# Kernel optimization log

Hardware: AMD Instinct MI355X
Metric: run time of the kernel (lower is better)

The kernel has to match this reference:

```python
import jax, jax.numpy as jnp
import numpy as np

# Directional rectangle cumulative max: max over the axis-aligned rectangle
# between each pixel and one image corner.

def _rectmax(x, rev_h, rev_w):
    y = jax.lax.cummax(x, axis=2, reverse=rev_h)
    return jax.lax.cummax(y, axis=3, reverse=rev_w)


def _guided_pool(xq, gq, rev_h, rev_w):
    # Guided landmark pool: each pixel takes max of itself and the directional
    # cumulative max restricted to guide==1 positions. With guide == ones this
    # reduces to the plain directional rectangle cummax (the un-guided pool).
    neg = jnp.finfo(xq.dtype).min
    masked = jnp.where(gq > 0, xq, neg)
    return jnp.maximum(xq, _rectmax(masked, rev_h, rev_w))

# (rev_h, rev_w) for TopLeft, TopRight, BottomLeft, BottomRight pools
_DIRS = [(True, True), (True, False), (False, True), (False, False)]


def setup_inputs() -> dict:
    key = jax.random.key(0)
    k1, k2, k3 = jax.random.split(key, 3)
    B, C, H, W = 16, 256, 64, 64
    Cout, K = 256, 3
    x = jax.random.normal(k1, (B, C, H, W), jnp.float32)
    weight = jax.random.normal(k2, (Cout, C, K, K), jnp.float32) * 0.02
    bias = jax.random.normal(k3, (Cout,), jnp.float32) * 0.02
    return {"x": x, "weight": weight, "bias": bias}


def reference(x, weight, bias):
    B, C, H, W = x.shape
    Q = C // 4
    # Original torch code squares x IN PLACE via chunk() views before pooling.
    xsq = x * x
    # Per-quadrant channel energy and its global (row, col) argmax -> one-hot guide.
    energy = xsq.reshape(B, 4, Q, H, W).sum(axis=2)            # [B,4,H,W]
    idx = jnp.argmax(energy.reshape(B, 4, H * W), axis=-1)     # [B,4]
    onehot = (jnp.arange(H * W) == idx[..., None]).astype(x.dtype)
    guide = jnp.broadcast_to(onehot.reshape(B, 4, 1, H, W), (B, 4, Q, H, W)).reshape(B, C, H, W)
    # Four directional guided pools, one per channel quadrant, then conv.
    xs = jnp.split(xsq, 4, axis=1)
    gs = jnp.split(guide, 4, axis=1)
    pooled = jnp.concatenate(
        [_guided_pool(xs[i], gs[i], *_DIRS[i]) for i in range(4)], axis=1)
    out = jax.lax.conv_general_dilated(
        pooled, weight, window_strides=(1, 1), padding='SAME',
        dimension_numbers=('NCHW', 'OIHW', 'NCHW'))
    return out + bias[None, :, None, None]
```

## Files before the change

### kernel.cpp

```cpp
#include <hip/hip_runtime.h>
#include <cstddef>

#define B_   16
#define C_   256
#define HW_  4096

typedef __attribute__((ext_vector_type(8)))  short bf16x8;
typedef __attribute__((ext_vector_type(16))) float f32x16;

static __device__ __forceinline__ unsigned short f2bf(float f) {
    unsigned int u = __float_as_uint(f);
    u += 0x7fffu + ((u >> 16) & 1u);
    return (unsigned short)(u >> 16);
}

__global__ __launch_bounds__(256) void fused_energy(const float* __restrict__ x,
                                                    unsigned short* __restrict__ xsqN,
                                                    float* __restrict__ pval,
                                                    int* __restrict__ pidx) {
    int blk = blockIdx.x;
    int b = blk >> 6, h = blk & 63;
    int tid = threadIdx.x;
    int w = tid & 63, layer = tid >> 6;
    __shared__ float earr[4][4][64];
    __shared__ unsigned short tile[64][264];
    float e0 = 0.f, e1 = 0.f, e2 = 0.f, e3 = 0.f;
    const float* xb = x + (size_t)b * C_ * HW_ + h * 64 + w;
#pragma unroll
    for (int i = 0; i < 8; ++i) {
        int c0 = (i * 4 + layer) * 8;
        union { unsigned short us[8]; int4 v; } u;
        float es = 0.f;
#pragma unroll
        for (int k = 0; k < 8; ++k) {
            float v = xb[(size_t)(c0 + k) * HW_];
            float s = v * v;
            es += s;
            u.us[k] = f2bf(s);
        }
        *(int4*)&tile[w][c0] = u.v;
        if ((i >> 1) == 0) e0 += es;
        else if ((i >> 1) == 1) e1 += es;
        else if ((i >> 1) == 2) e2 += es;
        else e3 += es;
    }
    earr[layer][0][w] = e0; earr[layer][1][w] = e1;
    earr[layer][2][w] = e2; earr[layer][3][w] = e3;
    __syncthreads();
    size_t base = (size_t)(b * 64 + h) * 64 * 256;
#pragma unroll
    for (int it = 0; it < 8; ++it) {
        int row  = it * 8 + (tid >> 5);
        int col8 = (tid & 31) * 8;
        *(int4*)(xsqN + base + (size_t)row * 256 + col8) = *(int4*)&tile[row][col8];
    }
    int q = tid >> 6;
    float ev = earr[0][q][w] + earr[1][q][w] + earr[2][q][w] + earr[3][q][w];
    int ix = h * 64 + w;
#pragma unroll
    for (int off = 32; off; off >>= 1) {
        float ov = __shfl_down(ev, off);
        int   oi = __shfl_down(ix, off);
        if (ov > ev || (ov == ev && oi < ix)) { ev = ov; ix = oi; }
    }
    if ((tid & 63) == 0) {
        pval[(b * 64 + h) * 4 + q] = ev;
        pidx[(b * 64 + h) * 4 + q] = ix;
    }
}

__global__ __launch_bounds__(64) void energy_final(const float* __restrict__ pval,
                                                   const int* __restrict__ pidx,
                                                   int* __restrict__ lm) {
    int bq = blockIdx.x;
    int b = bq >> 2, q = bq & 3;
    int h = threadIdx.x;
    float ev = pval[(b * 64 + h) * 4 + q];
    int   ix = pidx[(b * 64 + h) * 4 + q];
#pragma unroll
    for (int off = 32; off; off >>= 1) {
        float ov = __shfl_down(ev, off);
        int   oi = __shfl_down(ix, off);
        if (ov > ev || (ov == ev && oi < ix)) { ev = ov; ix = oi; }
    }
    if (h == 0) lm[bq] = ix;
}

__global__ __launch_bounds__(256) void lval_kernel(const unsigned short* __restrict__ xsqN,
                                                   const int* __restrict__ lm,
                                                   unsigned short* __restrict__ Lval) {
    int t = blockIdx.x * 256 + threadIdx.x;
    int b = t >> 8, c = t & 255, q = c >> 6;
    int l = lm[b * 4 + q];
    Lval[t] = xsqN[((size_t)((b * 64 + (l >> 6)) * 64 + (l & 63))) * 256 + c];
}

__global__ __launch_bounds__(64) void wt_pack(const float* __restrict__ w,
                                              unsigned short* __restrict__ wa) {
    int blk  = blockIdx.x;
    int lane = threadIdx.x;
    int cog = blk & 7;
    int s   = (blk >> 3) & 1;
    int cib = (blk >> 4) & 7;
    int j   = blk >> 7;
    int co  = cog * 32 + (lane & 31);
    int k0  = cib * 32 + s * 16 + (lane >> 5) * 8;
    union { unsigned short us[8]; int4 v; } u;
#pragma unroll
    for (int jj = 0; jj < 8; ++jj) {
        int ci = k0 + jj;
        u.us[jj] = f2bf(w[(size_t)(co * 256 + ci) * 9 + j]);
    }
    *(int4*)(wa + ((size_t)blk * 64 + lane) * 8) = u.v;
}

__global__ __launch_bounds__(512, 2) void conv_mfma(const unsigned short* __restrict__ xsqN,
                                                    const unsigned short* __restrict__ wa,
                                                    const float* __restrict__ bias,
                                                    const int* __restrict__ lm,
                                                    const unsigned short* __restrict__ Lval,
                                                    float* __restrict__ out) {
    int pt = blockIdx.x;
    int b  = pt >> 4;
    int h0 = (pt & 15) * 4;
    int tid  = threadIdx.x;
    int lane = tid & 63;
    int wv   = tid >> 6;
    int wy = wv >> 2, wx = wv & 3;
    int l31 = lane & 31, qh = lane >> 5;

    __shared__ unsigned short Bs[2][6 * 66 * 40];
    __shared__ unsigned short As[2][8192];

    f32x16 acc[4][2];
#pragma unroll
    for (int mt = 0; mt < 4; ++mt)
#pragma unroll
        for (int nt = 0; nt < 2; ++nt)
#pragma unroll
            for (int r = 0; r < 16; ++r) acc[mt][nt][r] = 0.f;

    int4 sv[4];
    int4 av0, av1;

    {
#pragma unroll
        for (int t2 = 0; t2 < 4; ++t2) {
            int idx = tid + t2 * 512;
            int4 v = {0, 0, 0, 0};
            if (idx < 1584) {
                int pr = idx / 264; int rem = idx - pr * 264;
                int pc = rem >> 2;  int part = rem & 3;
                int grow = h0 - 1 + pr, gcol = pc - 1;
                if ((unsigned)grow < 64u && (unsigned)gcol < 64u)
                    v = *(const int4*)(xsqN + (((size_t)(b * 64 + grow) * 64 + gcol) * 256 + part * 8));
            }
            sv[t2] = v;
        }
        int l = lm[b * 4 + 0];
        int hm = l >> 6, wm = l & 63;
#pragma unroll
        for (int t2 = 0; t2 < 4; ++t2) {
            int idx = tid + t2 * 512;
            if (idx < 1584) {
                int pr = idx / 264; int rem = idx - pr * 264;
                int pc = rem >> 2;  int part = rem & 3;
                int grow = h0 - 1 + pr, gcol = pc - 1;
                union { int4 v; unsigned short us[8]; } u; u.v = sv[t2];
                bool inb = ((unsigned)grow < 64u) && ((unsigned)gcol < 64u);
                if (inb && grow <= hm && gcol <= wm) {
                    union { int4 v; unsigned short us[8]; } Lu;
                    Lu.v = *(const int4*)(Lval + b * 256 + part * 8);
#pragma unroll
                    for (int k = 0; k < 8; ++k)
                        if (Lu.us[k] > u.us[k]) u.us[k] = Lu.us[k];
                }
                *(int4*)(&Bs[0][(pr * 66 + pc) * 40 + part * 8]) = u.v;
            }
        }
        const unsigned short* src = wa + tid * 16;
        av0 = *(const int4*)src;
        av1 = *(const int4*)(src + 8);
        *(int4*)(&As[0][tid * 16])     = av0;
        *(int4*)(&As[0][tid * 16 + 8]) = av1;
    }
    __syncthreads();

    for (int cib = 0; cib < 8; ++cib) {
        for (int j = 0; j < 9; ++j) {
            int p = cib * 9 + j;
            bool hasNext = (p < 71);
            if (hasNext) {
                int jn = j + 1, cibn = cib;
                if (jn == 9) { jn = 0; cibn = cib + 1; }
                const unsigned short* src = wa + ((size_t)(jn * 8 + cibn) << 13) + tid * 16;
                av0 = *(const int4*)src;
                av1 = *(const int4*)(src + 8);
            }
            if (j == 0 && cib < 7) {
                int nc = cib + 1;
#pragma unroll
                for (int t2 = 0; t2 < 4; ++t2) {
                    int idx = tid + t2 * 512;
                    int4 v = {0, 0, 0, 0};
                    if (idx < 1584) {
                        int pr = idx / 264; int rem = idx - pr * 264;
                        int pc = rem >> 2;  int part = rem & 3;
                        int grow = h0 - 1 + pr, gcol = pc - 1;
                        if ((unsigned)grow < 64u && (unsigned)gcol < 64u)
                            v = *(const int4*)(xsqN + (((size_t)(b * 64 + grow) * 64 + gcol) * 256 + nc * 32 + part * 8));
                    }
                    sv[t2] = v;
                }
            }

            {
                const unsigned short* Ab = &As[p & 1][0];
                const unsigned short* Bb = &Bs[cib & 1][0];
                int dh = j / 3 - 1, dw = j % 3 - 1;
                int r  = wx + dh + 1;
                int w0 = l31 + dw + 1;
#pragma unroll
                for (int s = 0; s < 2; ++s) {
                    const bf16x8* ap = (const bf16x8*)(Ab + (((s * 8 + wy * 4) * 64 + lane) << 3));
                    bf16x8 a0 = ap[0];
                    bf16x8 a1 = ap[64];
                    bf16x8 a2 = ap[128];
                    bf16x8 a3 = ap[192];
                    bf16x8 b0 = *(const bf16x8*)(Bb + (r * 66 + w0) * 40 + s * 16 + qh * 8);
                    bf16x8 b1 = *(const bf16x8*)(Bb + (r * 66 + w0 + 32) * 40 + s * 16 + qh * 8);
                    acc[0][0] = __builtin_amdgcn_mfma_f32_32x32x16_bf16(a0, b0, acc[0][0], 0, 0, 0);
                    acc[0][1] = __builtin_amdgcn_mfma_f32_32x32x16_bf16(a0, b1, acc[0][1], 0, 0, 0);
                    acc[1][0] = __builtin_amdgcn_mfma_f32_32x32x16_bf16(a1, b0, acc[1][0], 0, 0, 0);
                    acc[1][1] = __builtin_amdgcn_mfma_f32_32x32x16_bf16(a1, b1, acc[1][1], 0, 0, 0);
                    acc[2][0] = __builtin_amdgcn_mfma_f32_32x32x16_bf16(a2, b0, acc[2][0], 0, 0, 0);
                    acc[2][1] = __builtin_amdgcn_mfma_f32_32x32x16_bf16(a2, b1, acc[2][1], 0, 0, 0);
                    acc[3][0] = __builtin_amdgcn_mfma_f32_32x32x16_bf16(a3, b0, acc[3][0], 0, 0, 0);
                    acc[3][1] = __builtin_amdgcn_mfma_f32_32x32x16_bf16(a3, b1, acc[3][1], 0, 0, 0);
                }
            }

            if (j == 8 && cib < 7) {
                int nc = cib + 1;
                int l = lm[b * 4 + (nc >> 1)];
                int hm = l >> 6, wm = l & 63;
                bool qhle = (nc >> 1) < 2;
                bool qwle = ((nc >> 1) & 1) == 0;
                unsigned short* Bw = &Bs[(cib + 1) & 1][0];
#pragma unroll
                for (int t2 = 0; t2 < 4; ++t2) {
                    int idx = tid + t2 * 512;
                    if (idx < 1584) {
                        int pr = idx / 264; int rem = idx - pr * 264;
                        int pc = rem >> 2;  int part = rem & 3;
                        int grow = h0 - 1 + pr, gcol = pc - 1;
                        union { int4 v; unsigned short us[8]; } u; u.v = sv[t2];
                        bool inb = ((unsigned)grow < 64u) && ((unsigned)gcol < 64u);
                        bool hok = qhle ? (grow <= hm) : (grow >= hm);
                        bool wok = qwle ? (gcol <= wm) : (gcol >= wm);
                        if (inb && hok && wok) {
                            union { int4 v; unsigned short us[8]; } Lu;
                            Lu.v = *(const int4*)(Lval + b * 256 + nc * 32 + part * 8);
#pragma unroll
                            for (int k = 0; k < 8; ++k)
                                if (Lu.us[k] > u.us[k]) u.us[k] = Lu.us[k];
                        }
                        *(int4*)(&Bw[(pr * 66 + pc) * 40 + part * 8]) = u.v;
                    }
                }
            }
            if (hasNext) {
                unsigned short* dst = &As[(p + 1) & 1][tid * 16];
                *(int4*)dst       = av0;
                *(int4*)(dst + 8) = av1;
            }
            __syncthreads();
        }
    }

    int h = h0 + wx;
#pragma unroll
    for (int mt = 0; mt < 4; ++mt) {
#pragma unroll
        for (int nt = 0; nt < 2; ++nt) {
#pragma unroll
            for (int r = 0; r < 16; ++r) {
                int row = (r & 3) + 8 * (r >> 2) + 4 * qh;
                int co  = wy * 128 + mt * 32 + row;
                int w   = nt * 32 + l31;
                out[(((size_t)(b * 256 + co)) * 64 + h) * 64 + w] = acc[mt][nt][r] + bias[co];
            }
        }
    }
}

extern "C" void kernel_launch(void* const* d_in, const int* in_sizes, int n_in,
                              void* d_out, int out_size, void* d_ws, size_t ws_size,
                              hipStream_t stream) {
    const float* x      = (const float*)d_in[0];
    const float* weight = (const float*)d_in[1];
    const float* bias   = (const float*)d_in[2];
    float* out = (float*)d_out;

    char* ws = (char*)d_ws;
    int*            lmp  = (int*)ws;
    float*          pval = (float*)(ws + 256);
    int*            pidx = (int*)(ws + 256 + 16384);
    unsigned short* Lval = (unsigned short*)(ws + 256 + 32768);
    unsigned short* Wa   = (unsigned short*)(ws + 49152);
    unsigned short* xsqN = (unsigned short*)(ws + 49152 + 1179648);

    hipLaunchKernelGGL(fused_energy, dim3(1024), dim3(256), 0, stream, x, xsqN, pval, pidx);
    hipLaunchKernelGGL(energy_final, dim3(64), dim3(64), 0, stream, pval, pidx, lmp);
    hipLaunchKernelGGL(lval_kernel, dim3(16), dim3(256), 0, stream, xsqN, lmp, Lval);
    hipLaunchKernelGGL(wt_pack, dim3(1152), dim3(64), 0, stream, weight, Wa);
    hipLaunchKernelGGL(conv_mfma, dim3(256), dim3(512), 0, stream, xsqN, Wa, bias, lmp, Lval, out);
}
```

Before: 198.5 us.

## Retile conv to 8-row blocks with weights in registers and fewer barriers

Restructures the implicit-GEMM conv so each block covers 8 image rows and half the output channels. Each of 4 waves computes a 128x128 tile (4x4 MFMA accumulators), and the A (weight) fragments are read directly from global memory into registers with one-step prefetch instead of being staged through LDS. The 9 taps per channel block now run without a barrier between them, leaving one __syncthreads per channel block rather than one per tap. The lval kernel is also folded into energy_final to save a launch. In exchange the kernel needs more registers per wave and a larger LDS halo buffer, and runs at 256 threads with launch bounds for one block per SIMD, which lowers occupancy.

```diff
diff --git a/kernel.cpp b/kernel.cpp
--- a/kernel.cpp
+++ b/kernel.cpp
@@ -71,28 +71,25 @@
 
 __global__ __launch_bounds__(64) void energy_final(const float* __restrict__ pval,
                                                    const int* __restrict__ pidx,
-                                                   int* __restrict__ lm) {
+                                                   const unsigned short* __restrict__ xsqN,
+                                                   int* __restrict__ lm,
+                                                   unsigned short* __restrict__ Lval) {
     int bq = blockIdx.x;
     int b = bq >> 2, q = bq & 3;
-    int h = threadIdx.x;
-    float ev = pval[(b * 64 + h) * 4 + q];
-    int   ix = pidx[(b * 64 + h) * 4 + q];
+    int t = threadIdx.x;
+    float ev = pval[(b * 64 + t) * 4 + q];
+    int   ix = pidx[(b * 64 + t) * 4 + q];
 #pragma unroll
     for (int off = 32; off; off >>= 1) {
         float ov = __shfl_down(ev, off);
         int   oi = __shfl_down(ix, off);
         if (ov > ev || (ov == ev && oi < ix)) { ev = ov; ix = oi; }
     }
-    if (h == 0) lm[bq] = ix;
-}
-
-__global__ __launch_bounds__(256) void lval_kernel(const unsigned short* __restrict__ xsqN,
-                                                   const int* __restrict__ lm,
-                                                   unsigned short* __restrict__ Lval) {
-    int t = blockIdx.x * 256 + threadIdx.x;
-    int b = t >> 8, c = t & 255, q = c >> 6;
-    int l = lm[b * 4 + q];
-    Lval[t] = xsqN[((size_t)((b * 64 + (l >> 6)) * 64 + (l & 63))) * 256 + c];
+    int ixw = __shfl(ix, 0);
+    if (t == 0) lm[bq] = ixw;
+    int hm = ixw >> 6, wm = ixw & 63;
+    Lval[b * 256 + q * 64 + t] =
+        xsqN[((size_t)((b * 64 + hm) * 64 + wm)) * 256 + q * 64 + t];
 }
 
 __global__ __launch_bounds__(64) void wt_pack(const float* __restrict__ w,
@@ -114,44 +111,44 @@
     *(int4*)(wa + ((size_t)blk * 64 + lane) * 8) = u.v;
 }
 
-__global__ __launch_bounds__(512, 2) void conv_mfma(const unsigned short* __restrict__ xsqN,
+__global__ __launch_bounds__(256, 1) void conv_mfma(const unsigned short* __restrict__ xsqN,
                                                     const unsigned short* __restrict__ wa,
                                                     const float* __restrict__ bias,
                                                     const int* __restrict__ lm,
                                                     const unsigned short* __restrict__ Lval,
                                                     float* __restrict__ out) {
     int pt = blockIdx.x;
-    int b  = pt >> 4;
-    int h0 = (pt & 15) * 4;
+    int b   = pt >> 4;
+    int hb  = (pt >> 1) & 7;
+    int wy  = pt & 1;
+    int h0g = hb * 8;
     int tid  = threadIdx.x;
     int lane = tid & 63;
-    int wv   = tid >> 6;
-    int wy = wv >> 2, wx = wv & 3;
+    int wx   = tid >> 6;
     int l31 = lane & 31, qh = lane >> 5;
 
-    __shared__ unsigned short Bs[2][6 * 66 * 40];
-    __shared__ unsigned short As[2][8192];
-
-    f32x16 acc[4][2];
+    __shared__ unsigned short Bs[2][26400];
+
+    f32x16 acc[4][4];
 #pragma unroll
     for (int mt = 0; mt < 4; ++mt)
 #pragma unroll
-        for (int nt = 0; nt < 2; ++nt)
+        for (int nt = 0; nt < 4; ++nt)
 #pragma unroll
             for (int r = 0; r < 16; ++r) acc[mt][nt][r] = 0.f;
 
-    int4 sv[4];
-    int4 av0, av1;
+    int4 sv[11];
+    int4 aC[8], aN[8];
 
     {
 #pragma unroll
-        for (int t2 = 0; t2 < 4; ++t2) {
-            int idx = tid + t2 * 512;
+        for (int t2 = 0; t2 < 11; ++t2) {
+            int idx = tid + t2 * 256;
             int4 v = {0, 0, 0, 0};
-            if (idx < 1584) {
+            if (idx < 2640) {
                 int pr = idx / 264; int rem = idx - pr * 264;
                 int pc = rem >> 2;  int part = rem & 3;
-                int grow = h0 - 1 + pr, gcol = pc - 1;
+                int grow = h0g - 1 + pr, gcol = pc - 1;
                 if ((unsigned)grow < 64u && (unsigned)gcol < 64u)
                     v = *(const int4*)(xsqN + (((size_t)(b * 64 + grow) * 64 + gcol) * 256 + part * 8));
             }
@@ -160,12 +157,12 @@
         int l = lm[b * 4 + 0];
         int hm = l >> 6, wm = l & 63;
 #pragma unroll
-        for (int t2 = 0; t2 < 4; ++t2) {
-            int idx = tid + t2 * 512;
-            if (idx < 1584) {
+        for (int t2 = 0; t2 < 11; ++t2) {
+            int idx = tid + t2 * 256;
+            if (idx < 2640) {
                 int pr = idx / 264; int rem = idx - pr * 264;
                 int pc = rem >> 2;  int part = rem & 3;
-                int grow = h0 - 1 + pr, gcol = pc - 1;
+                int grow = h0g - 1 + pr, gcol = pc - 1;
                 union { int4 v; unsigned short us[8]; } u; u.v = sv[t2];
                 bool inb = ((unsigned)grow < 64u) && ((unsigned)gcol < 64u);
                 if (inb && grow <= hm && gcol <= wm) {
@@ -178,116 +175,121 @@
                 *(int4*)(&Bs[0][(pr * 66 + pc) * 40 + part * 8]) = u.v;
             }
         }
-        const unsigned short* src = wa + tid * 16;
-        av0 = *(const int4*)src;
-        av1 = *(const int4*)(src + 8);
-        *(int4*)(&As[0][tid * 16])     = av0;
-        *(int4*)(&As[0][tid * 16 + 8]) = av1;
+#pragma unroll
+        for (int s = 0; s < 2; ++s)
+#pragma unroll
+            for (int mt = 0; mt < 4; ++mt)
+                aC[s * 4 + mt] = *(const int4*)(wa + (((s * 8 + wy * 4 + mt) * 64 + lane) << 3));
     }
     __syncthreads();
 
     for (int cib = 0; cib < 8; ++cib) {
+        if (cib < 7) {
+            int nc = cib + 1;
+#pragma unroll
+            for (int t2 = 0; t2 < 11; ++t2) {
+                int idx = tid + t2 * 256;
+                int4 v = {0, 0, 0, 0};
+                if (idx < 2640) {
+                    int pr = idx / 264; int rem = idx - pr * 264;
+                    int pc = rem >> 2;  int part = rem & 3;
+                    int grow = h0g - 1 + pr, gcol = pc - 1;
+                    if ((unsigned)grow < 64u && (unsigned)gcol < 64u)
+                        v = *(const int4*)(xsqN + (((size_t)(b * 64 + grow) * 64 + gcol) * 256 + nc * 32 + part * 8));
+                }
+                sv[t2] = v;
+            }
+        }
+
+        const unsigned short* Bb = &Bs[cib & 1][0];
+#pragma unroll
         for (int j = 0; j < 9; ++j) {
-            int p = cib * 9 + j;
-            bool hasNext = (p < 71);
+            bool hasNext = !(j == 8 && cib == 7);
             if (hasNext) {
-                int jn = j + 1, cibn = cib;
-                if (jn == 9) { jn = 0; cibn = cib + 1; }
-                const unsigned short* src = wa + ((size_t)(jn * 8 + cibn) << 13) + tid * 16;
-                av0 = *(const int4*)src;
-                av1 = *(const int4*)(src + 8);
-            }
-            if (j == 0 && cib < 7) {
-                int nc = cib + 1;
-#pragma unroll
-                for (int t2 = 0; t2 < 4; ++t2) {
-                    int idx = tid + t2 * 512;
-                    int4 v = {0, 0, 0, 0};
-                    if (idx < 1584) {
-                        int pr = idx / 264; int rem = idx - pr * 264;
-                        int pc = rem >> 2;  int part = rem & 3;
-                        int grow = h0 - 1 + pr, gcol = pc - 1;
-                        if ((unsigned)grow < 64u && (unsigned)gcol < 64u)
-                            v = *(const int4*)(xsqN + (((size_t)(b * 64 + grow) * 64 + gcol) * 256 + nc * 32 + part * 8));
+                int jn = (j == 8) ? 0 : j + 1;
+                int cibn = (j == 8) ? cib + 1 : cib;
+                const unsigned short* an = wa + ((size_t)(jn * 8 + cibn) << 13);
+#pragma unroll
+                for (int s = 0; s < 2; ++s)
+#pragma unroll
+                    for (int mt = 0; mt < 4; ++mt)
+                        aN[s * 4 + mt] = *(const int4*)(an + (((s * 8 + wy * 4 + mt) * 64 + lane) << 3));
+            }
+            int dh = j / 3 - 1, dw = j % 3 - 1;
+            int row0 = 2 * wx + dh + 1;
+            int w0 = l31 + dw + 1;
+            bf16x8 bf[8];
+#pragma unroll
+            for (int s = 0; s < 2; ++s)
+#pragma unroll
+                for (int rp = 0; rp < 2; ++rp)
+#pragma unroll
+                    for (int nc2 = 0; nc2 < 2; ++nc2)
+                        bf[(s << 2) | (rp << 1) | nc2] =
+                            *(const bf16x8*)(Bb + ((row0 + rp) * 66 + w0 + nc2 * 32) * 40 + s * 16 + qh * 8);
+#pragma unroll
+            for (int s = 0; s < 2; ++s) {
+#pragma unroll
+                for (int mt = 0; mt < 4; ++mt) {
+                    bf16x8 af = *(const bf16x8*)&aC[s * 4 + mt];
+#pragma unroll
+                    for (int rp = 0; rp < 2; ++rp)
+#pragma unroll
+                        for (int nc2 = 0; nc2 < 2; ++nc2) {
+                            int nt = rp * 2 + nc2;
+                            acc[mt][nt] = __builtin_amdgcn_mfma_f32_32x32x16_bf16(
+                                af, bf[(s << 2) | (rp << 1) | nc2], acc[mt][nt], 0, 0, 0);
+                        }
+                }
+            }
+            if (hasNext) {
+#pragma unroll
+                for (int k = 0; k < 8; ++k) aC[k] = aN[k];
+            }
+        }
+
+        if (cib < 7) {
+            int nc = cib + 1;
+            int l = lm[b * 4 + (nc >> 1)];
+            int hm = l >> 6, wm = l & 63;
+            bool qhle = (nc >> 1) < 2;
+            bool qwle = ((nc >> 1) & 1) == 0;
+            unsigned short* Bw = &Bs[(cib + 1) & 1][0];
+#pragma unroll
+            for (int t2 = 0; t2 < 11; ++t2) {
+                int idx = tid + t2 * 256;
+                if (idx < 2640) {
+                    int pr = idx / 264; int rem = idx - pr * 264;
+                    int pc = rem >> 2;  int part = rem & 3;
+                    int grow = h0g - 1 + pr, gcol = pc - 1;
+                    union { int4 v; unsigned short us[8]; } u; u.v = sv[t2];
+                    bool inb = ((unsigned)grow < 64u) && ((unsigned)gcol < 64u);
+                    bool hok = qhle ? (grow <= hm) : (grow >= hm);
+                    bool wok = qwle ? (gcol <= wm) : (gcol >= wm);
+                    if (inb && hok && wok) {
+                        union { int4 v; unsigned short us[8]; } Lu;
+                        Lu.v = *(const int4*)(Lval + b * 256 + nc * 32 + part * 8);
+#pragma unroll
+                        for (int k = 0; k < 8; ++k)
+                            if (Lu.us[k] > u.us[k]) u.us[k] = Lu.us[k];
                     }
-                    sv[t2] = v;
+                    *(int4*)(&Bw[(pr * 66 + pc) * 40 + part * 8]) = u.v;
                 }
             }
-
-            {
-                const unsigned short* Ab = &As[p & 1][0];
-                const unsigned short* Bb = &Bs[cib & 1][0];
-                int dh = j / 3 - 1, dw = j % 3 - 1;
-                int r  = wx + dh + 1;
-                int w0 = l31 + dw + 1;
-#pragma unroll
-                for (int s = 0; s < 2; ++s) {
-                    const bf16x8* ap = (const bf16x8*)(Ab + (((s * 8 + wy * 4) * 64 + lane) << 3));
-                    bf16x8 a0 = ap[0];
-                    bf16x8 a1 = ap[64];
-                    bf16x8 a2 = ap[128];
-                    bf16x8 a3 = ap[192];
-                    bf16x8 b0 = *(const bf16x8*)(Bb + (r * 66 + w0) * 40 + s * 16 + qh * 8);
-                    bf16x8 b1 = *(const bf16x8*)(Bb + (r * 66 + w0 + 32) * 40 + s * 16 + qh * 8);
-                    acc[0][0] = __builtin_amdgcn_mfma_f32_32x32x16_bf16(a0, b0, acc[0][0], 0, 0, 0);
-                    acc[0][1] = __builtin_amdgcn_mfma_f32_32x32x16_bf16(a0, b1, acc[0][1], 0, 0, 0);
-                    acc[1][0] = __builtin_amdgcn_mfma_f32_32x32x16_bf16(a1, b0, acc[1][0], 0, 0, 0);
-                    acc[1][1] = __builtin_amdgcn_mfma_f32_32x32x16_bf16(a1, b1, acc[1][1], 0, 0, 0);
-                    acc[2][0] = __builtin_amdgcn_mfma_f32_32x32x16_bf16(a2, b0, acc[2][0], 0, 0, 0);
-                    acc[2][1] = __builtin_amdgcn_mfma_f32_32x32x16_bf16(a2, b1, acc[2][1], 0, 0, 0);
-                    acc[3][0] = __builtin_amdgcn_mfma_f32_32x32x16_bf16(a3, b0, acc[3][0], 0, 0, 0);
-                    acc[3][1] = __builtin_amdgcn_mfma_f32_32x32x16_bf16(a3, b1, acc[3][1], 0, 0, 0);
-                }
-            }
-
-            if (j == 8 && cib < 7) {
-                int nc = cib + 1;
-                int l = lm[b * 4 + (nc >> 1)];
-                int hm = l >> 6, wm = l & 63;
-                bool qhle = (nc >> 1) < 2;
-                bool qwle = ((nc >> 1) & 1) == 0;
-                unsigned short* Bw = &Bs[(cib + 1) & 1][0];
-#pragma unroll
-                for (int t2 = 0; t2 < 4; ++t2) {
-                    int idx = tid + t2 * 512;
-                    if (idx < 1584) {
-                        int pr = idx / 264; int rem = idx - pr * 264;
-                        int pc = rem >> 2;  int part = rem & 3;
-                        int grow = h0 - 1 + pr, gcol = pc - 1;
-                        union { int4 v; unsigned short us[8]; } u; u.v = sv[t2];
-                        bool inb = ((unsigned)grow < 64u) && ((unsigned)gcol < 64u);
-                        bool hok = qhle ? (grow <= hm) : (grow >= hm);
-                        bool wok = qwle ? (gcol <= wm) : (gcol >= wm);
-                        if (inb && hok && wok) {
-                            union { int4 v; unsigned short us[8]; } Lu;
-                            Lu.v = *(const int4*)(Lval + b * 256 + nc * 32 + part * 8);
-#pragma unroll
-                            for (int k = 0; k < 8; ++k)
-                                if (Lu.us[k] > u.us[k]) u.us[k] = Lu.us[k];
-                        }
-                        *(int4*)(&Bw[(pr * 66 + pc) * 40 + part * 8]) = u.v;
-                    }
-                }
-            }
-            if (hasNext) {
-                unsigned short* dst = &As[(p + 1) & 1][tid * 16];
-                *(int4*)dst       = av0;
-                *(int4*)(dst + 8) = av1;
-            }
-            __syncthreads();
-        }
-    }
-
-    int h = h0 + wx;
+        }
+        __syncthreads();
+    }
+
 #pragma unroll
     for (int mt = 0; mt < 4; ++mt) {
 #pragma unroll
-        for (int nt = 0; nt < 2; ++nt) {
+        for (int nt = 0; nt < 4; ++nt) {
+            int h = h0g + 2 * wx + (nt >> 1);
+            int w = (nt & 1) * 32 + l31;
 #pragma unroll
             for (int r = 0; r < 16; ++r) {
                 int row = (r & 3) + 8 * (r >> 2) + 4 * qh;
                 int co  = wy * 128 + mt * 32 + row;
-                int w   = nt * 32 + l31;
                 out[(((size_t)(b * 256 + co)) * 64 + h) * 64 + w] = acc[mt][nt][r] + bias[co];
             }
         }
@@ -311,8 +313,7 @@
     unsigned short* xsqN = (unsigned short*)(ws + 49152 + 1179648);
 
     hipLaunchKernelGGL(fused_energy, dim3(1024), dim3(256), 0, stream, x, xsqN, pval, pidx);
-    hipLaunchKernelGGL(energy_final, dim3(64), dim3(64), 0, stream, pval, pidx, lmp);
-    hipLaunchKernelGGL(lval_kernel, dim3(16), dim3(256), 0, stream, xsqN, lmp, Lval);
+    hipLaunchKernelGGL(energy_final, dim3(64), dim3(64), 0, stream, pval, pidx, xsqN, lmp, Lval);
     hipLaunchKernelGGL(wt_pack, dim3(1152), dim3(64), 0, stream, weight, Wa);
-    hipLaunchKernelGGL(conv_mfma, dim3(256), dim3(512), 0, stream, xsqN, Wa, bias, lmp, Lval, out);
-}
+    hipLaunchKernelGGL(conv_mfma, dim3(256), dim3(256), 0, stream, xsqN, Wa, bias, lmp, Lval, out);
+}
```

After: 410.0 us. +106.6%, slower.
